# Kernel tuning notes

Measured on AMD Instinct MI355X. Metric: run time of the kernel, lower is better.

The kernel has to match this reference:

```python
import jax, jax.numpy as jnp
import numpy as np

N_NODES = 100000
N_EDGES = 1600000
D = 64          # embedding_dim (in_feats == out_feats)
H = 1           # num_heads
NEG_SLOPE = 0.2


def setup_inputs() -> dict:
    key = jax.random.key(0)
    k = jax.random.split(key, 7)
    feat = jax.random.normal(k[0], (N_NODES, D), dtype=jnp.float32)
    W = jax.random.normal(k[1], (D, H * D), dtype=jnp.float32) * (1.0 / np.sqrt(D))
    attn_l = jax.random.normal(k[2], (1, H, D), dtype=jnp.float32) * (1.0 / np.sqrt(D))
    attn_r = jax.random.normal(k[3], (1, H, D), dtype=jnp.float32) * (1.0 / np.sqrt(D))
    bias = jnp.zeros((H * D,), dtype=jnp.float32)
    src = jax.random.randint(k[4], (N_EDGES,), 0, N_NODES, dtype=jnp.int32)
    dst = jax.random.randint(k[5], (N_EDGES,), 0, N_NODES, dtype=jnp.int32)
    return {"feat": feat, "W": W, "attn_l": attn_l, "attn_r": attn_r,
            "bias": bias, "src": src, "dst": dst}


def reference(feat, W, attn_l, attn_r, bias, src, dst):
    # fc (no bias), view to [N, H, D_out]
    ft = (feat @ W).reshape(-1, H, D)                       # [N, H, D]
    # per-node attention halves
    el = jnp.sum(ft * attn_l, axis=-1, keepdims=True)       # [N, H, 1]
    er = jnp.sum(ft * attn_r, axis=-1, keepdims=True)       # [N, H, 1]
    # edge score: u_add_v then leaky_relu
    e = el[src] + er[dst]                                    # [E, H, 1]
    e = jnp.where(e > 0, e, NEG_SLOPE * e)
    # edge softmax over incoming edges of each destination node
    emax = jax.ops.segment_max(e, dst, num_segments=N_NODES)  # [N, H, 1]
    e_exp = jnp.exp(e - emax[dst])
    denom = jax.ops.segment_sum(e_exp, dst, num_segments=N_NODES)  # [N, H, 1]
    a = e_exp / denom[dst]                                   # [E, H, 1]
    # u_mul_e + sum aggregation to destination
    m = ft[src] * a                                          # [E, H, D]
    rst = jax.ops.segment_sum(m, dst, num_segments=N_NODES)  # [N, H, D]
    # residual (Identity since in_feats == out_feats) + bias
    rst = rst + feat.reshape(-1, H, D)
    rst = rst + bias.reshape(1, H, D)
    return rst
```

## Files before the change

### kernel.cpp

```cpp
#include <hip/hip_runtime.h>
#include <hip/hip_fp16.h>
#include <math.h>

#define NN 100000
#define NE 1600000
#define D 64
#define NEG_SLOPE 0.2f
#define NBKT 391
#define NBIN 391
#define CHUNKB 4096
#define BSLOT 5120
#define NTILE 1563

typedef __attribute__((ext_vector_type(8))) short short8;
typedef __attribute__((ext_vector_type(4))) float f32x4;

template<int CTRL>
__device__ __forceinline__ float dpp_add(float x) {
    int y = __builtin_amdgcn_update_dpp(0, __float_as_int(x), CTRL, 0xf, 0xf, true);
    return x + __int_as_float(y);
}
__device__ __forceinline__ float wave_sum63(float x) {
    x = dpp_add<0x111>(x); x = dpp_add<0x112>(x); x = dpp_add<0x114>(x);
    x = dpp_add<0x118>(x); x = dpp_add<0x142>(x); x = dpp_add<0x143>(x);
    return x;
}
__device__ __forceinline__ float rdlane_f(float v, int l) {
    return __int_as_float(__builtin_amdgcn_readlane(__float_as_int(v), l));
}
__device__ __forceinline__ unsigned bf16_1(float f) {
    unsigned x = __float_as_uint(f);
    return (x + 0x7fffu + ((x >> 16) & 1u)) >> 16;
}
__device__ __forceinline__ unsigned bfpack(float a, float b) {
    return bf16_1(a) | (bf16_1(b) << 16);
}

__global__ __launch_bounds__(256) void k_bg(
    const int* __restrict__ src, const int* __restrict__ dst,
    unsigned* __restrict__ bcnt, unsigned* __restrict__ binned,
    const float* __restrict__ feat, const float* __restrict__ W,
    const float* __restrict__ attn_l, const float* __restrict__ attn_r,
    float* __restrict__ el, float* __restrict__ er)
{
    __shared__ __align__(16) char smem[1664];
    int t = threadIdx.x;

    if (blockIdx.x < NBIN) {
        unsigned* lh = (unsigned*)smem;
        unsigned b0 = blockIdx.x * CHUNKB;
        unsigned b1 = min(b0 + CHUNKB, (unsigned)NE);
        if (b0 >= b1) return;
        unsigned n4 = (b1 - b0) >> 2;
        for (int k = t; k < NBKT; k += 256) lh[k] = 0u;
        __syncthreads();
        const int4* d4 = (const int4*)(dst + b0);
        const int4* s4 = (const int4*)(src + b0);
        for (unsigned i = t; i < n4; i += 256) {
            int4 v = d4[i];
            atomicAdd(&lh[((unsigned)v.x) >> 8], 1u);
            atomicAdd(&lh[((unsigned)v.y) >> 8], 1u);
            atomicAdd(&lh[((unsigned)v.z) >> 8], 1u);
            atomicAdd(&lh[((unsigned)v.w) >> 8], 1u);
        }
        __syncthreads();
        for (int k = t; k < NBKT; k += 256) {
            unsigned c = lh[k];
            if (c) lh[k] = (unsigned)k * BSLOT + atomicAdd(&bcnt[k], c);
        }
        __syncthreads();
        for (unsigned i = t; i < n4; i += 256) {
            int4 dv = d4[i];
            int4 sv = s4[i];
            { unsigned d_=(unsigned)dv.x, s_=(unsigned)sv.x;
              unsigned pos=atomicAdd(&lh[d_>>8],1u); binned[pos]=(s_<<8)|(d_&255u); }
            { unsigned d_=(unsigned)dv.y, s_=(unsigned)sv.y;
              unsigned pos=atomicAdd(&lh[d_>>8],1u); binned[pos]=(s_<<8)|(d_&255u); }
            { unsigned d_=(unsigned)dv.z, s_=(unsigned)sv.z;
              unsigned pos=atomicAdd(&lh[d_>>8],1u); binned[pos]=(s_<<8)|(d_&255u); }
            { unsigned d_=(unsigned)dv.w, s_=(unsigned)sv.w;
              unsigned pos=atomicAdd(&lh[d_>>8],1u); binned[pos]=(s_<<8)|(d_&255u); }
        }
        return;
    }

    float* wlS = (float*)smem;
    float* wrS = (float*)(smem + 256);
    int n0 = (int)(blockIdx.x - NBIN) * 64;
    {
        int k = t >> 2, s = t & 3;
        float pl = 0.f, pr = 0.f;
        #pragma unroll
        for (int q = 0; q < 4; ++q) {
            int seg = s + q * 4;
            float4 f = *(const float4*)(W + k * 64 + seg * 4);
            float4 a = *(const float4*)(attn_l + seg * 4);
            float4 b = *(const float4*)(attn_r + seg * 4);
            pl += f.x*a.x + f.y*a.y + f.z*a.z + f.w*a.w;
            pr += f.x*b.x + f.y*b.y + f.z*b.z + f.w*b.w;
        }
        pl += __shfl_xor(pl, 1, 64); pl += __shfl_xor(pl, 2, 64);
        pr += __shfl_xor(pr, 1, 64); pr += __shfl_xor(pr, 2, 64);
        if (s == 0) { wlS[k] = pl; wrS[k] = pr; }
    }
    __syncthreads();
    {
        int r = t >> 2, s = t & 3;
        int n = n0 + r;
        bool valid = n < NN;
        const float* fp = feat + (size_t)(valid ? n : (NN - 1)) * D;
        float pl = 0.f, pr = 0.f;
        #pragma unroll
        for (int q = 0; q < 4; ++q) {
            int seg = s + q * 4;
            float4 f = *(const float4*)(fp + seg * 4);
            float4 a = *(const float4*)(wlS + seg * 4);
            float4 b = *(const float4*)(wrS + seg * 4);
            pl += f.x*a.x + f.y*a.y + f.z*a.z + f.w*a.w;
            pr += f.x*b.x + f.y*b.y + f.z*b.z + f.w*b.w;
        }
        pl += __shfl_xor(pl, 1, 64); pl += __shfl_xor(pl, 2, 64);
        pr += __shfl_xor(pr, 1, 64); pr += __shfl_xor(pr, 2, 64);
        if (s == 0 && valid) { el[n] = pl; er[n] = pr; }
    }
}

__global__ __launch_bounds__(256) void k_sg(
    const unsigned* __restrict__ bcnt, const unsigned* __restrict__ binned,
    const float* __restrict__ el, const float* __restrict__ er,
    int* __restrict__ perm, float* __restrict__ eperm, uint2* __restrict__ rowBE,
    const float* __restrict__ feat, const float* __restrict__ W,
    __half* __restrict__ ft)
{
    __shared__ __align__(16) char smem[22784];
    int t = threadIdx.x;

    if (blockIdx.x < NBKT) {
        unsigned* lh    = (unsigned*)smem;
        unsigned* cur   = (unsigned*)smem + 256;
        unsigned* stage = (unsigned*)smem + 512;
        int b = blockIdx.x;
        unsigned beg = (unsigned)b * BSLOT;
        unsigned cnt = min(bcnt[b], (unsigned)BSLOT);
        lh[t] = 0u;
        __syncthreads();
        for (unsigned i = t; i < cnt; i += 256) {
            unsigned w = binned[beg + i];
            stage[i] = w;
            atomicAdd(&lh[w & 255u], 1u);
        }
        __syncthreads();
        for (int off = 1; off < 256; off <<= 1) {
            unsigned u = (t >= off) ? lh[t - off] : 0u;
            __syncthreads();
            lh[t] += u;
            __syncthreads();
        }
        unsigned start = (t == 0) ? 0u : lh[t - 1];
        unsigned node = ((unsigned)b << 8) + (unsigned)t;
        if (node < NN) {
            uint2 be; be.x = beg + start; be.y = beg + lh[t];
            rowBE[node] = be;
        }
        cur[t] = start;
        __syncthreads();
        for (unsigned i = t; i < cnt; i += 256) {
            unsigned w = stage[i];
            unsigned dl = w & 255u;
            unsigned pos = atomicAdd(&cur[dl], 1u);
            unsigned sj = w >> 8;
            float e = el[sj] + er[((unsigned)b << 8) + dl];
            e = e > 0.0f ? e : NEG_SLOPE * e;
            perm[beg + pos] = (int)sj;
            eperm[beg + pos] = __expf(e);
        }
        __syncthreads();
        if (t < 8 && cnt + t < BSLOT) {
            perm[beg + cnt + t] = 0;
            eperm[beg + cnt + t] = 0.0f;
        }
        return;
    }

    unsigned short* Ab = (unsigned short*)smem;
    unsigned short* Bb = (unsigned short*)(smem + 8192);
    int n0 = (int)(blockIdx.x - NBKT) * 64;
    {
        int j = t & 63, g = t >> 6;
        unsigned m = (unsigned)((j & 7) << 4);
        #pragma unroll
        for (int i = 0; i < 8; ++i) {
            int k0 = g * 16 + i * 2;
            float w0 = W[k0 * 64 + j];
            float w1 = W[(k0 + 1) * 64 + j];
            *(unsigned*)((char*)Bb + j * 128 + (((unsigned)(k0 * 2)) ^ m)) = bfpack(w0, w1);
        }
    }
    {
        int r = t >> 2, s = t & 3;
        int n = n0 + r;
        bool valid = n < NN;
        const float* fp = feat + (size_t)(valid ? n : (NN - 1)) * D;
        unsigned m = (unsigned)((r & 7) << 4);
        #pragma unroll
        for (int q = 0; q < 4; ++q) {
            int seg = s + q * 4;
            float4 f = *(const float4*)(fp + seg * 4);
            uint2 pk;
            pk.x = bfpack(f.x, f.y);
            pk.y = bfpack(f.z, f.w);
            *(uint2*)((char*)Ab + r * 128 + (((unsigned)(seg * 8)) ^ m)) = pk;
        }
    }
    __syncthreads();

    int w = t >> 6, l = t & 63;
    int lr = l & 15, lg = l >> 4;
    f32x4 acc0 = {0.f,0.f,0.f,0.f};
    f32x4 acc1 = {0.f,0.f,0.f,0.f};
    f32x4 acc2 = {0.f,0.f,0.f,0.f};
    f32x4 acc3 = {0.f,0.f,0.f,0.f};

    int jrow = w * 16 + lr;
    unsigned bm = (unsigned)((jrow & 7) << 4);
    short8 bf0 = *(const short8*)((char*)Bb + jrow * 128 + (((unsigned)(0 + lg * 16)) ^ bm));
    short8 bf1 = *(const short8*)((char*)Bb + jrow * 128 + (((unsigned)(64 + lg * 16)) ^ bm));

    #pragma unroll
    for (int rt = 0; rt < 4; ++rt) {
        int arow = rt * 16 + lr;
        unsigned am = (unsigned)((arow & 7) << 4);
        short8 a0 = *(const short8*)((char*)Ab + arow * 128 + (((unsigned)(0 + lg * 16)) ^ am));
        short8 a1 = *(const short8*)((char*)Ab + arow * 128 + (((unsigned)(64 + lg * 16)) ^ am));
        f32x4 acc = (rt == 0) ? acc0 : (rt == 1) ? acc1 : (rt == 2) ? acc2 : acc3;
        acc = __builtin_amdgcn_mfma_f32_16x16x32_bf16(a0, bf0, acc, 0, 0, 0);
        acc = __builtin_amdgcn_mfma_f32_16x16x32_bf16(a1, bf1, acc, 0, 0, 0);
        if (rt == 0) acc0 = acc; else if (rt == 1) acc1 = acc;
        else if (rt == 2) acc2 = acc; else acc3 = acc;
    }

    int col = w * 16 + lr;
    #pragma unroll
    for (int rt = 0; rt < 4; ++rt) {
        f32x4 acc = (rt == 0) ? acc0 : (rt == 1) ? acc1 : (rt == 2) ? acc2 : acc3;
        #pragma unroll
        for (int i = 0; i < 4; ++i) {
            int row = rt * 16 + lg * 4 + i;
            int nn = n0 + row;
            if (nn < NN) ft[(size_t)nn * D + col] = __float2half(acc[i]);
        }
    }
}

__device__ __noinline__ void agg_node64(int d, int lane, unsigned beg, unsigned end,
                                        const int* __restrict__ perm,
                                        const float* __restrict__ eperm,
                                        const __half* __restrict__ ft,
                                        const float* __restrict__ feat,
                                        const float* __restrict__ bias,
                                        float* __restrict__ out) {
    float s = 0.0f;
    for (unsigned base = beg; base < end; base += 64) {
        unsigned i = base + lane;
        float exx = (i < end) ? eperm[i] : 0.0f;
        s += rdlane_f(wave_sum63(exx), 63);
    }
    float inv_s = __frcp_rn(s);
    float acc = 0.0f;
    for (unsigned jj = beg; jj < end; ++jj) {
        int sj = perm[jj];
        float wj = eperm[jj];
        acc = fmaf(__half2float(ft[((size_t)(unsigned)sj << 6) + lane]), wj, acc);
    }
    acc *= inv_s;
    out[(size_t)d * D + lane] = acc + feat[(size_t)d * D + lane] + bias[lane];
}

#define LOAD8(B, J) do { \
    int _s0 = ps[(J)+0]; int _s1 = ps[(J)+1]; int _s2 = ps[(J)+2]; int _s3 = ps[(J)+3]; \
    int _s4 = ps[(J)+4]; int _s5 = ps[(J)+5]; int _s6 = ps[(J)+6]; int _s7 = ps[(J)+7]; \
    B##0 = *(const __half*)(ftb + (((size_t)(unsigned)_s0) << 7) + lb); \
    B##1 = *(const __half*)(ftb + (((size_t)(unsigned)_s1) << 7) + lb); \
    B##2 = *(const __half*)(ftb + (((size_t)(unsigned)_s2) << 7) + lb); \
    B##3 = *(const __half*)(ftb + (((size_t)(unsigned)_s3) << 7) + lb); \
    B##4 = *(const __half*)(ftb + (((size_t)(unsigned)_s4) << 7) + lb); \
    B##5 = *(const __half*)(ftb + (((size_t)(unsigned)_s5) << 7) + lb); \
    B##6 = *(const __half*)(ftb + (((size_t)(unsigned)_s6) << 7) + lb); \
    B##7 = *(const __half*)(ftb + (((size_t)(unsigned)_s7) << 7) + lb); \
} while (0)

#define FMA8(B, J) do { \
    acc = fmaf(__half2float(B##0), rdlane_f(ex, (J) + 0), acc); \
    acc = fmaf(__half2float(B##1), rdlane_f(ex, (J) + 1), acc); \
    acc = fmaf(__half2float(B##2), rdlane_f(ex, (J) + 2), acc); \
    acc = fmaf(__half2float(B##3), rdlane_f(ex, (J) + 3), acc); \
    acc = fmaf(__half2float(B##4), rdlane_f(ex, (J) + 4), acc); \
    acc = fmaf(__half2float(B##5), rdlane_f(ex, (J) + 5), acc); \
    acc = fmaf(__half2float(B##6), rdlane_f(ex, (J) + 6), acc); \
    acc = fmaf(__half2float(B##7), rdlane_f(ex, (J) + 7), acc); \
} while (0)

__global__ __launch_bounds__(256) void k_agg(const uint2* __restrict__ rowBE,
                                             const int* __restrict__ perm,
                                             const float* __restrict__ eperm,
                                             const __half* __restrict__ ft,
                                             const float* __restrict__ feat,
                                             const float* __restrict__ bias,
                                             float* __restrict__ out) {
    int gid = blockIdx.x * 256 + threadIdx.x;
    int d = gid >> 6;
    int lane = gid & 63;
    if (d >= NN) return;

    uint2 be = rowBE[d];
    unsigned beg = be.x;
    int deg = (int)(be.y - be.x);

    if (deg > 64) {
        agg_node64(d, lane, be.x, be.y, perm, eperm, ft, feat, bias, out);
        return;
    }
    if (deg == 0) {
        out[(size_t)d * D + lane] = feat[(size_t)d * D + lane] + bias[lane];
        return;
    }

    float ex = (lane < deg) ? eperm[beg + lane] : 0.0f;
    float fv = feat[(size_t)d * D + lane];
    float bv = bias[lane];

    unsigned begu = __builtin_amdgcn_readfirstlane(beg);
    int degu = __builtin_amdgcn_readfirstlane(deg);
    const int* ps = perm + begu;
    const char* ftb = (const char*)ft;
    size_t lb = (size_t)((unsigned)lane << 1);

    __half c0, c1, c2, c3, c4, c5, c6, c7;
    __half n0, n1, n2, n3, n4, n5, n6, n7;
    LOAD8(c, 0);

    float s = rdlane_f(wave_sum63(ex), 63);
    float inv_s = __frcp_rn(s);

    float acc = 0.0f;
    int j = 0;
    while (true) {
        bool more = (j + 8) < degu;
        if (more) LOAD8(n, j + 8);
        FMA8(c, j);
        j += 8;
        if (!more) break;
        bool more2 = (j + 8) < degu;
        if (more2) LOAD8(c, j + 8);
        FMA8(n, j);
        j += 8;
        if (!more2) break;
    }
    acc *= inv_s;
    out[(size_t)d * D + lane] = acc + fv + bv;
}

extern "C" void kernel_launch(void* const* d_in, const int* in_sizes, int n_in,
                              void* d_out, int out_size, void* d_ws, size_t ws_size,
                              hipStream_t stream) {
    const float* feat   = (const float*)d_in[0];
    const float* W      = (const float*)d_in[1];
    const float* attn_l = (const float*)d_in[2];
    const float* attn_r = (const float*)d_in[3];
    const float* bias   = (const float*)d_in[4];
    const int*   src    = (const int*)d_in[5];
    const int*   dst    = (const int*)d_in[6];
    float* out = (float*)d_out;

    char* ws = (char*)d_ws;
    __half*   ft     = (__half*)(ws);
    float*    el     = (float*)(ws + 12800000);
    float*    er     = (float*)(ws + 13200000);
    int*      perm   = (int*)(ws + 13600000);
    uint2*    rowBE  = (uint2*)(ws + 21607680);
    unsigned* bcnt   = (unsigned*)(ws + 22407680);
    unsigned* binned = (unsigned*)(ws + 22409248);
    float*    eperm  = (float*)binned;

    hipMemsetAsync(bcnt, 0, NBKT * sizeof(unsigned), stream);
    k_bg<<<NBIN + NTILE, 256, 0, stream>>>(src, dst, bcnt, binned,
                                           feat, W, attn_l, attn_r, el, er);
    k_sg<<<NBKT + NTILE, 256, 0, stream>>>(bcnt, binned, el, er,
                                           perm, eperm, rowBE, feat, W, ft);
    k_agg<<<(NN * 64 + 255) / 256, 256, 0, stream>>>(rowBE, perm, eperm,
                                                     ft, feat, bias, out);
}
```

Measured before the change: 102.9 us.

## Restructure pipeline: move el/er into GEMM tiles, split edge-exp into separate kernel

The el/er attention projections move out of the binning kernel and into the feature-GEMM tiles of k_sg, so feat is read once per tile for both the ft projection and the attention halves. Because el is then not ready during the sort, the sort only writes a packed perm entry holding the local destination in the high bits and the source in the low 17 bits. A new k_eperm kernel then computes the exponentiated scores, and the aggregation masks the source index back out. The memset becomes a tiny zero kernel. This adds two kernel launches and an extra pass over perm in exchange for shorter dependency chains and one fewer read of feat.

```diff
diff --git a/kernel.cpp b/kernel.cpp
--- a/kernel.cpp
+++ b/kernel.cpp
@@ -11,6 +11,7 @@
 #define CHUNKB 4096
 #define BSLOT 5120
 #define NTILE 1563
+#define SMASK 131071
 
 typedef __attribute__((ext_vector_type(8))) short short8;
 typedef __attribute__((ext_vector_type(4))) float f32x4;
@@ -36,101 +37,58 @@
     return bf16_1(a) | (bf16_1(b) << 16);
 }
 
-__global__ __launch_bounds__(256) void k_bg(
-    const int* __restrict__ src, const int* __restrict__ dst,
-    unsigned* __restrict__ bcnt, unsigned* __restrict__ binned,
+__global__ __launch_bounds__(256) void k_zero(unsigned* __restrict__ bcnt) {
+    int i = blockIdx.x * 256 + threadIdx.x;
+    if (i < NBKT) bcnt[i] = 0u;
+}
+
+__global__ __launch_bounds__(256) void k_bin(const int* __restrict__ src,
+                                             const int* __restrict__ dst,
+                                             unsigned* __restrict__ bcnt,
+                                             unsigned* __restrict__ binned) {
+    __shared__ unsigned lh[NBKT];
+    int t = threadIdx.x;
+    unsigned b0 = blockIdx.x * CHUNKB;
+    unsigned b1 = min(b0 + CHUNKB, (unsigned)NE);
+    if (b0 >= b1) return;
+    unsigned n4 = (b1 - b0) >> 2;
+    for (int k = t; k < NBKT; k += 256) lh[k] = 0u;
+    __syncthreads();
+    const int4* d4 = (const int4*)(dst + b0);
+    const int4* s4 = (const int4*)(src + b0);
+    for (unsigned i = t; i < n4; i += 256) {
+        int4 v = d4[i];
+        atomicAdd(&lh[((unsigned)v.x) >> 8], 1u);
+        atomicAdd(&lh[((unsigned)v.y) >> 8], 1u);
+        atomicAdd(&lh[((unsigned)v.z) >> 8], 1u);
+        atomicAdd(&lh[((unsigned)v.w) >> 8], 1u);
+    }
+    __syncthreads();
+    for (int k = t; k < NBKT; k += 256) {
+        unsigned c = lh[k];
+        if (c) lh[k] = (unsigned)k * BSLOT + atomicAdd(&bcnt[k], c);
+    }
+    __syncthreads();
+    for (unsigned i = t; i < n4; i += 256) {
+        int4 dv = d4[i];
+        int4 sv = s4[i];
+        { unsigned d_=(unsigned)dv.x, s_=(unsigned)sv.x;
+          unsigned pos=atomicAdd(&lh[d_>>8],1u); binned[pos]=(s_<<8)|(d_&255u); }
+        { unsigned d_=(unsigned)dv.y, s_=(unsigned)sv.y;
+          unsigned pos=atomicAdd(&lh[d_>>8],1u); binned[pos]=(s_<<8)|(d_&255u); }
+        { unsigned d_=(unsigned)dv.z, s_=(unsigned)sv.z;
+          unsigned pos=atomicAdd(&lh[d_>>8],1u); binned[pos]=(s_<<8)|(d_&255u); }
+        { unsigned d_=(unsigned)dv.w, s_=(unsigned)sv.w;
+          unsigned pos=atomicAdd(&lh[d_>>8],1u); binned[pos]=(s_<<8)|(d_&255u); }
+    }
+}
+
+__global__ __launch_bounds__(256) void k_sg(
+    const unsigned* __restrict__ bcnt, const unsigned* __restrict__ binned,
+    int* __restrict__ perm, uint2* __restrict__ rowBE,
     const float* __restrict__ feat, const float* __restrict__ W,
     const float* __restrict__ attn_l, const float* __restrict__ attn_r,
-    float* __restrict__ el, float* __restrict__ er)
-{
-    __shared__ __align__(16) char smem[1664];
-    int t = threadIdx.x;
-
-    if (blockIdx.x < NBIN) {
-        unsigned* lh = (unsigned*)smem;
-        unsigned b0 = blockIdx.x * CHUNKB;
-        unsigned b1 = min(b0 + CHUNKB, (unsigned)NE);
-        if (b0 >= b1) return;
-        unsigned n4 = (b1 - b0) >> 2;
-        for (int k = t; k < NBKT; k += 256) lh[k] = 0u;
-        __syncthreads();
-        const int4* d4 = (const int4*)(dst + b0);
-        const int4* s4 = (const int4*)(src + b0);
-        for (unsigned i = t; i < n4; i += 256) {
-            int4 v = d4[i];
-            atomicAdd(&lh[((unsigned)v.x) >> 8], 1u);
-            atomicAdd(&lh[((unsigned)v.y) >> 8], 1u);
-            atomicAdd(&lh[((unsigned)v.z) >> 8], 1u);
-            atomicAdd(&lh[((unsigned)v.w) >> 8], 1u);
-        }
-        __syncthreads();
-        for (int k = t; k < NBKT; k += 256) {
-            unsigned c = lh[k];
-            if (c) lh[k] = (unsigned)k * BSLOT + atomicAdd(&bcnt[k], c);
-        }
-        __syncthreads();
-        for (unsigned i = t; i < n4; i += 256) {
-            int4 dv = d4[i];
-            int4 sv = s4[i];
-            { unsigned d_=(unsigned)dv.x, s_=(unsigned)sv.x;
-              unsigned pos=atomicAdd(&lh[d_>>8],1u); binned[pos]=(s_<<8)|(d_&255u); }
-            { unsigned d_=(unsigned)dv.y, s_=(unsigned)sv.y;
-              unsigned pos=atomicAdd(&lh[d_>>8],1u); binned[pos]=(s_<<8)|(d_&255u); }
-            { unsigned d_=(unsigned)dv.z, s_=(unsigned)sv.z;
-              unsigned pos=atomicAdd(&lh[d_>>8],1u); binned[pos]=(s_<<8)|(d_&255u); }
-            { unsigned d_=(unsigned)dv.w, s_=(unsigned)sv.w;
-              unsigned pos=atomicAdd(&lh[d_>>8],1u); binned[pos]=(s_<<8)|(d_&255u); }
-        }
-        return;
-    }
-
-    float* wlS = (float*)smem;
-    float* wrS = (float*)(smem + 256);
-    int n0 = (int)(blockIdx.x - NBIN) * 64;
-    {
-        int k = t >> 2, s = t & 3;
-        float pl = 0.f, pr = 0.f;
-        #pragma unroll
-        for (int q = 0; q < 4; ++q) {
-            int seg = s + q * 4;
-            float4 f = *(const float4*)(W + k * 64 + seg * 4);
-            float4 a = *(const float4*)(attn_l + seg * 4);
-            float4 b = *(const float4*)(attn_r + seg * 4);
-            pl += f.x*a.x + f.y*a.y + f.z*a.z + f.w*a.w;
-            pr += f.x*b.x + f.y*b.y + f.z*b.z + f.w*b.w;
-        }
-        pl += __shfl_xor(pl, 1, 64); pl += __shfl_xor(pl, 2, 64);
-        pr += __shfl_xor(pr, 1, 64); pr += __shfl_xor(pr, 2, 64);
-        if (s == 0) { wlS[k] = pl; wrS[k] = pr; }
-    }
-    __syncthreads();
-    {
-        int r = t >> 2, s = t & 3;
-        int n = n0 + r;
-        bool valid = n < NN;
-        const float* fp = feat + (size_t)(valid ? n : (NN - 1)) * D;
-        float pl = 0.f, pr = 0.f;
-        #pragma unroll
-        for (int q = 0; q < 4; ++q) {
-            int seg = s + q * 4;
-            float4 f = *(const float4*)(fp + seg * 4);
-            float4 a = *(const float4*)(wlS + seg * 4);
-            float4 b = *(const float4*)(wrS + seg * 4);
-            pl += f.x*a.x + f.y*a.y + f.z*a.z + f.w*a.w;
-            pr += f.x*b.x + f.y*b.y + f.z*b.z + f.w*b.w;
-        }
-        pl += __shfl_xor(pl, 1, 64); pl += __shfl_xor(pl, 2, 64);
-        pr += __shfl_xor(pr, 1, 64); pr += __shfl_xor(pr, 2, 64);
-        if (s == 0 && valid) { el[n] = pl; er[n] = pr; }
-    }
-}
-
-__global__ __launch_bounds__(256) void k_sg(
-    const unsigned* __restrict__ bcnt, const unsigned* __restrict__ binned,
-    const float* __restrict__ el, const float* __restrict__ er,
-    int* __restrict__ perm, float* __restrict__ eperm, uint2* __restrict__ rowBE,
-    const float* __restrict__ feat, const float* __restrict__ W,
-    __half* __restrict__ ft)
+    __half* __restrict__ ft, float* __restrict__ el, float* __restrict__ er)
 {
     __shared__ __align__(16) char smem[22784];
     int t = threadIdx.x;
@@ -168,23 +126,33 @@
             unsigned w = stage[i];
             unsigned dl = w & 255u;
             unsigned pos = atomicAdd(&cur[dl], 1u);
-            unsigned sj = w >> 8;
-            float e = el[sj] + er[((unsigned)b << 8) + dl];
-            e = e > 0.0f ? e : NEG_SLOPE * e;
-            perm[beg + pos] = (int)sj;
-            eperm[beg + pos] = __expf(e);
-        }
-        __syncthreads();
-        if (t < 8 && cnt + t < BSLOT) {
-            perm[beg + cnt + t] = 0;
-            eperm[beg + cnt + t] = 0.0f;
+            perm[beg + pos] = (int)((dl << 17) | (w >> 8));
         }
         return;
     }
 
     unsigned short* Ab = (unsigned short*)smem;
     unsigned short* Bb = (unsigned short*)(smem + 8192);
+    float* wlS = (float*)(smem + 16384);
+    float* wrS = (float*)(smem + 16640);
     int n0 = (int)(blockIdx.x - NBKT) * 64;
+
+    {
+        int k = t >> 2, s = t & 3;
+        float pl = 0.f, pr = 0.f;
+        #pragma unroll
+        for (int q = 0; q < 4; ++q) {
+            int seg = s + q * 4;
+            float4 f = *(const float4*)(W + k * 64 + seg * 4);
+            float4 a = *(const float4*)(attn_l + seg * 4);
+            float4 b = *(const float4*)(attn_r + seg * 4);
+            pl += f.x*a.x + f.y*a.y + f.z*a.z + f.w*a.w;
+            pr += f.x*b.x + f.y*b.y + f.z*b.z + f.w*b.w;
+        }
+        pl += __shfl_xor(pl, 1, 64); pl += __shfl_xor(pl, 2, 64);
+        pr += __shfl_xor(pr, 1, 64); pr += __shfl_xor(pr, 2, 64);
+        if (s == 0) { wlS[k] = pl; wrS[k] = pr; }
+    }
     {
         int j = t & 63, g = t >> 6;
         unsigned m = (unsigned)((j & 7) << 4);
@@ -196,21 +164,30 @@
             *(unsigned*)((char*)Bb + j * 128 + (((unsigned)(k0 * 2)) ^ m)) = bfpack(w0, w1);
         }
     }
+    __syncthreads();
     {
         int r = t >> 2, s = t & 3;
         int n = n0 + r;
         bool valid = n < NN;
         const float* fp = feat + (size_t)(valid ? n : (NN - 1)) * D;
+        float pl = 0.f, pr = 0.f;
         unsigned m = (unsigned)((r & 7) << 4);
         #pragma unroll
         for (int q = 0; q < 4; ++q) {
             int seg = s + q * 4;
             float4 f = *(const float4*)(fp + seg * 4);
+            float4 a = *(const float4*)(wlS + seg * 4);
+            float4 b = *(const float4*)(wrS + seg * 4);
+            pl += f.x*a.x + f.y*a.y + f.z*a.z + f.w*a.w;
+            pr += f.x*b.x + f.y*b.y + f.z*b.z + f.w*b.w;
             uint2 pk;
             pk.x = bfpack(f.x, f.y);
             pk.y = bfpack(f.z, f.w);
             *(uint2*)((char*)Ab + r * 128 + (((unsigned)(seg * 8)) ^ m)) = pk;
         }
+        pl += __shfl_xor(pl, 1, 64); pl += __shfl_xor(pl, 2, 64);
+        pr += __shfl_xor(pr, 1, 64); pr += __shfl_xor(pr, 2, 64);
+        if (s == 0 && valid) { el[n] = pl; er[n] = pr; }
     }
     __syncthreads();
 
@@ -248,6 +225,30 @@
             int row = rt * 16 + lg * 4 + i;
             int nn = n0 + row;
             if (nn < NN) ft[(size_t)nn * D + col] = __float2half(acc[i]);
+        }
+    }
+}
+
+__global__ __launch_bounds__(256) void k_eperm(const unsigned* __restrict__ bcnt,
+                                               const int* __restrict__ perm,
+                                               const float* __restrict__ el,
+                                               const float* __restrict__ er,
+                                               float* __restrict__ eperm) {
+    int g = blockIdx.x;
+    int b = g >> 2, q = g & 3;
+    unsigned base = (unsigned)b * BSLOT;
+    unsigned cnt = min(bcnt[b], (unsigned)BSLOT);
+    unsigned lo = (unsigned)q * 1280u;
+    unsigned hi = min(lo + 1280u, min(cnt + 8u, (unsigned)BSLOT));
+    unsigned erbase = (unsigned)b << 8;
+    for (unsigned i = lo + threadIdx.x; i < hi; i += 256) {
+        if (i < cnt) {
+            unsigned p = (unsigned)perm[base + i];
+            float e = el[p & SMASK] + er[erbase + (p >> 17)];
+            e = e > 0.f ? e : NEG_SLOPE * e;
+            eperm[base + i] = __expf(e);
+        } else {
+            eperm[base + i] = 0.0f;
         }
     }
 }
@@ -268,7 +269,7 @@
     float inv_s = __frcp_rn(s);
     float acc = 0.0f;
     for (unsigned jj = beg; jj < end; ++jj) {
-        int sj = perm[jj];
+        int sj = perm[jj] & SMASK;
         float wj = eperm[jj];
         acc = fmaf(__half2float(ft[((size_t)(unsigned)sj << 6) + lane]), wj, acc);
     }
@@ -277,8 +278,10 @@
 }
 
 #define LOAD8(B, J) do { \
-    int _s0 = ps[(J)+0]; int _s1 = ps[(J)+1]; int _s2 = ps[(J)+2]; int _s3 = ps[(J)+3]; \
-    int _s4 = ps[(J)+4]; int _s5 = ps[(J)+5]; int _s6 = ps[(J)+6]; int _s7 = ps[(J)+7]; \
+    int _s0 = ps[(J)+0] & SMASK; int _s1 = ps[(J)+1] & SMASK; \
+    int _s2 = ps[(J)+2] & SMASK; int _s3 = ps[(J)+3] & SMASK; \
+    int _s4 = ps[(J)+4] & SMASK; int _s5 = ps[(J)+5] & SMASK; \
+    int _s6 = ps[(J)+6] & SMASK; int _s7 = ps[(J)+7] & SMASK; \
     B##0 = *(const __half*)(ftb + (((size_t)(unsigned)_s0) << 7) + lb); \
     B##1 = *(const __half*)(ftb + (((size_t)(unsigned)_s1) << 7) + lb); \
     B##2 = *(const __half*)(ftb + (((size_t)(unsigned)_s2) << 7) + lb); \
@@ -380,13 +383,13 @@
     uint2*    rowBE  = (uint2*)(ws + 21607680);
     unsigned* bcnt   = (unsigned*)(ws + 22407680);
     unsigned* binned = (unsigned*)(ws + 22409248);
-    float*    eperm  = (float*)binned;
-
-    hipMemsetAsync(bcnt, 0, NBKT * sizeof(unsigned), stream);
-    k_bg<<<NBIN + NTILE, 256, 0, stream>>>(src, dst, bcnt, binned,
-                                           feat, W, attn_l, attn_r, el, er);
-    k_sg<<<NBKT + NTILE, 256, 0, stream>>>(bcnt, binned, el, er,
-                                           perm, eperm, rowBE, feat, W, ft);
+    float*    eperm  = (float*)(ws + 30416928);
+
+    k_zero<<<2, 256, 0, stream>>>(bcnt);
+    k_bin<<<NBIN, 256, 0, stream>>>(src, dst, bcnt, binned);
+    k_sg<<<NBKT + NTILE, 256, 0, stream>>>(bcnt, binned, perm, rowBE,
+                                           feat, W, attn_l, attn_r, ft, el, er);
+    k_eperm<<<NBKT * 4, 256, 0, stream>>>(bcnt, perm, el, er, eperm);
     k_agg<<<(NN * 64 + 255) / 256, 256, 0, stream>>>(rowBE, perm, eperm,
                                                      ft, feat, bias, out);
 }
```

After: 97.46 us. 1.06x faster.
